# Performance work log

Hardware: AMD Instinct MI355X
Metric: run time of the kernel (lower is better)

The kernel has to match this reference:

```python
import jax, jax.numpy as jnp
import numpy as np

E = 100000          # number of edges
IN_FEATS = 256      # in_edge_feats
HIDDEN = 128        # hidden_size
K = 16              # neighbors per edge (uniform-degree rendering of ragged lists)


def setup_inputs() -> dict:
    key = jax.random.key(0)
    k1, k2, k3, k4 = jax.random.split(key, 4)
    edge_feats = jax.random.normal(k1, (E, IN_FEATS), dtype=jnp.float32)
    neighbors = jax.random.randint(k2, (E, K), 0, E, dtype=jnp.int32)
    # Linear params (torch Linear: y = x @ W^T + b; here W stored as [in, out])
    W = jax.random.normal(k3, (IN_FEATS, HIDDEN), dtype=jnp.float32) / np.sqrt(IN_FEATS)
    b = jax.random.normal(k4, (HIDDEN,), dtype=jnp.float32) * 0.01
    return {"edge_feats": edge_feats, "neighbors": neighbors, "W": W, "b": b}


def reference(edge_feats, neighbors, W, b):
    # Dense linear transform of all edge features: [E, H]
    t = edge_feats @ W + b
    # Gather each edge's K neighbor transformed features and sum: [E, K, H] -> [E, H]
    nbr_sum = jnp.take(t, neighbors, axis=0).sum(axis=1)
    # agg[i] = t[i] + sum_{n in neighbors[i]} t[n]
    return t + nbr_sum
```

## Files before the change

kernel.cpp:

```cpp
#include <hip/hip_runtime.h>
#include <hip/hip_bf16.h>
#include <stdint.h>

#define E_EDGES 100000
#define IN_F    256
#define HID     128
#define KNB     16

typedef short bf16x8 __attribute__((ext_vector_type(8)));
typedef float f32x4  __attribute__((ext_vector_type(4)));

__device__ __forceinline__ unsigned short f2bf(float f) {
    union { float f; unsigned u; } v; v.f = f;
    unsigned u = v.u;
    u += 0x7fffu + ((u >> 16) & 1u);
    return (unsigned short)(u >> 16);
}

__global__ void conv_w_kernel(const float* __restrict__ W, unsigned short* __restrict__ Wt) {
    int t = blockIdx.x * blockDim.x + threadIdx.x;
    int n = t & (HID - 1);
    int k = t >> 7;
    Wt[(size_t)n * IN_F + k] = f2bf(W[(size_t)k * HID + n]);
}

__launch_bounds__(256)
__global__ void gemm_t_kernel(const float* __restrict__ A,
                              const unsigned short* __restrict__ Wt,
                              const float* __restrict__ bias,
                              unsigned short* __restrict__ T) {
    const int wave = threadIdx.x >> 6;
    const int lane = threadIdx.x & 63;
    const int l15  = lane & 15;
    const int quad = lane >> 4;
    const int row0 = blockIdx.x * 32;
    const int col0 = wave * 32;

    f32x4 acc[2][2] = {};

    for (int k0 = 0; k0 < IN_F; k0 += 32) {
        bf16x8 afrag[2], bfrag[2];
        #pragma unroll
        for (int rt = 0; rt < 2; ++rt) {
            const float* ap = A + (size_t)(row0 + rt * 16 + l15) * IN_F + k0 + quad * 8;
            float4 lo = *(const float4*)ap;
            float4 hi = *(const float4*)(ap + 4);
            bf16x8 f;
            f[0] = (short)f2bf(lo.x); f[1] = (short)f2bf(lo.y);
            f[2] = (short)f2bf(lo.z); f[3] = (short)f2bf(lo.w);
            f[4] = (short)f2bf(hi.x); f[5] = (short)f2bf(hi.y);
            f[6] = (short)f2bf(hi.z); f[7] = (short)f2bf(hi.w);
            afrag[rt] = f;
        }
        #pragma unroll
        for (int ct = 0; ct < 2; ++ct) {
            const unsigned short* bp =
                Wt + (size_t)(col0 + ct * 16 + l15) * IN_F + k0 + quad * 8;
            bfrag[ct] = *(const bf16x8*)bp;
        }
        #pragma unroll
        for (int rt = 0; rt < 2; ++rt)
            #pragma unroll
            for (int ct = 0; ct < 2; ++ct)
                acc[rt][ct] = __builtin_amdgcn_mfma_f32_16x16x32_bf16(
                    afrag[rt], bfrag[ct], acc[rt][ct], 0, 0, 0);
    }

    #pragma unroll
    for (int rt = 0; rt < 2; ++rt) {
        #pragma unroll
        for (int ct = 0; ct < 2; ++ct) {
            const int col = col0 + ct * 16 + l15;
            const float bv = bias[col];
            #pragma unroll
            for (int i = 0; i < 4; ++i) {
                const int row = row0 + rt * 16 + quad * 4 + i;
                T[(size_t)row * HID + col] = f2bf(acc[rt][ct][i] + bv);
            }
        }
    }
}

__launch_bounds__(256)
__global__ void gather_sum_kernel(const unsigned short* __restrict__ T,
                                  const int* __restrict__ nbr,
                                  float* __restrict__ out) {
    __shared__ int sidx[256];
    const int tid   = threadIdx.x;
    const int edge0 = blockIdx.x * 16;
    sidx[tid] = nbr[(size_t)edge0 * KNB + tid];
    __syncthreads();

    const int el   = tid >> 4;
    const int lane = tid & 15;
    const int edge = edge0 + el;

    float acc[8];
    {
        uint4 v = *(const uint4*)(T + (size_t)edge * HID + lane * 8);
        unsigned w[4] = { v.x, v.y, v.z, v.w };
        union { unsigned u; float f; } c;
        #pragma unroll
        for (int j = 0; j < 4; ++j) {
            c.u = w[j] << 16;          acc[2 * j]     = c.f;
            c.u = w[j] & 0xffff0000u;  acc[2 * j + 1] = c.f;
        }
    }
    #pragma unroll
    for (int k = 0; k < KNB; ++k) {
        const int n = sidx[el * KNB + k];
        uint4 v = *(const uint4*)(T + (size_t)n * HID + lane * 8);
        unsigned w[4] = { v.x, v.y, v.z, v.w };
        union { unsigned u; float f; } c;
        #pragma unroll
        for (int j = 0; j < 4; ++j) {
            c.u = w[j] << 16;          acc[2 * j]     += c.f;
            c.u = w[j] & 0xffff0000u;  acc[2 * j + 1] += c.f;
        }
    }

    float* op = out + (size_t)edge * HID + lane * 8;
    float4 o0 = { acc[0], acc[1], acc[2], acc[3] };
    float4 o1 = { acc[4], acc[5], acc[6], acc[7] };
    *(float4*)op       = o0;
    *(float4*)(op + 4) = o1;
}

extern "C" void kernel_launch(void* const* d_in, const int* in_sizes, int n_in,
                              void* d_out, int out_size, void* d_ws, size_t ws_size,
                              hipStream_t stream) {
    const float* edge_feats = (const float*)d_in[0];
    const int*   neighbors  = (const int*)d_in[1];
    const float* W          = (const float*)d_in[2];
    const float* b          = (const float*)d_in[3];
    float*       out        = (float*)d_out;

    unsigned short* Wt = (unsigned short*)d_ws;
    unsigned short* T  = (unsigned short*)d_ws + (size_t)IN_F * HID;

    conv_w_kernel<<<(IN_F * HID) / 256, 256, 0, stream>>>(W, Wt);
    gemm_t_kernel<<<E_EDGES / 32, 256, 0, stream>>>(edge_feats, Wt, b, T);
    gather_sum_kernel<<<E_EDGES / 16, 256, 0, stream>>>(T, neighbors, out);
}
```

Before: 271.5 us.

## Restructure GEMM so each wave owns 16 rows across all columns, prefetching A

The GEMM tiling changes so that each wave computes a 16-row strip over all 128 output columns instead of a 32x32 tile. Every A element is now loaded and converted to bf16 exactly once rather than once per column-wave, and the whole A row slice is prefetched into registers up front to hide load latency. The cost is that each wave reads all of Wt, and the 16-entry float4 prefetch plus 8 accumulators raise register pressure. Bounds guards for the new 64-row block size are added.

```diff
diff --git a/kernel.cpp b/kernel.cpp
--- a/kernel.cpp
+++ b/kernel.cpp
@@ -33,50 +33,48 @@
     const int lane = threadIdx.x & 63;
     const int l15  = lane & 15;
     const int quad = lane >> 4;
-    const int row0 = blockIdx.x * 32;
-    const int col0 = wave * 32;
+    const int rowbase = blockIdx.x * 64 + wave * 16;
 
-    f32x4 acc[2][2] = {};
+    int arow = rowbase + l15;
+    if (arow >= E_EDGES) arow = E_EDGES - 1;
 
-    for (int k0 = 0; k0 < IN_F; k0 += 32) {
-        bf16x8 afrag[2], bfrag[2];
+    const float* ap = A + (size_t)arow * IN_F + quad * 8;
+    float4 apre[16];
+    #pragma unroll
+    for (int k0 = 0; k0 < 8; ++k0) {
+        apre[2 * k0]     = *(const float4*)(ap + k0 * 32);
+        apre[2 * k0 + 1] = *(const float4*)(ap + k0 * 32 + 4);
+    }
+
+    f32x4 acc[8] = {};
+
+    #pragma unroll
+    for (int k0 = 0; k0 < 8; ++k0) {
+        bf16x8 bfrag[8];
         #pragma unroll
-        for (int rt = 0; rt < 2; ++rt) {
-            const float* ap = A + (size_t)(row0 + rt * 16 + l15) * IN_F + k0 + quad * 8;
-            float4 lo = *(const float4*)ap;
-            float4 hi = *(const float4*)(ap + 4);
-            bf16x8 f;
-            f[0] = (short)f2bf(lo.x); f[1] = (short)f2bf(lo.y);
-            f[2] = (short)f2bf(lo.z); f[3] = (short)f2bf(lo.w);
-            f[4] = (short)f2bf(hi.x); f[5] = (short)f2bf(hi.y);
-            f[6] = (short)f2bf(hi.z); f[7] = (short)f2bf(hi.w);
-            afrag[rt] = f;
-        }
+        for (int ct = 0; ct < 8; ++ct)
+            bfrag[ct] = *(const bf16x8*)(Wt + (size_t)(ct * 16 + l15) * IN_F
+                                            + k0 * 32 + quad * 8);
+        float4 lo = apre[2 * k0], hi = apre[2 * k0 + 1];
+        bf16x8 af;
+        af[0] = (short)f2bf(lo.x); af[1] = (short)f2bf(lo.y);
+        af[2] = (short)f2bf(lo.z); af[3] = (short)f2bf(lo.w);
+        af[4] = (short)f2bf(hi.x); af[5] = (short)f2bf(hi.y);
+        af[6] = (short)f2bf(hi.z); af[7] = (short)f2bf(hi.w);
         #pragma unroll
-        for (int ct = 0; ct < 2; ++ct) {
-            const unsigned short* bp =
-                Wt + (size_t)(col0 + ct * 16 + l15) * IN_F + k0 + quad * 8;
-            bfrag[ct] = *(const bf16x8*)bp;
-        }
-        #pragma unroll
-        for (int rt = 0; rt < 2; ++rt)
-            #pragma unroll
-            for (int ct = 0; ct < 2; ++ct)
-                acc[rt][ct] = __builtin_amdgcn_mfma_f32_16x16x32_bf16(
-                    afrag[rt], bfrag[ct], acc[rt][ct], 0, 0, 0);
+        for (int ct = 0; ct < 8; ++ct)
+            acc[ct] = __builtin_amdgcn_mfma_f32_16x16x32_bf16(af, bfrag[ct], acc[ct], 0, 0, 0);
     }
 
     #pragma unroll
-    for (int rt = 0; rt < 2; ++rt) {
+    for (int ct = 0; ct < 8; ++ct) {
+        const int col = ct * 16 + l15;
+        const float bv = bias[col];
         #pragma unroll
-        for (int ct = 0; ct < 2; ++ct) {
-            const int col = col0 + ct * 16 + l15;
-            const float bv = bias[col];
-            #pragma unroll
-            for (int i = 0; i < 4; ++i) {
-                const int row = row0 + rt * 16 + quad * 4 + i;
-                T[(size_t)row * HID + col] = f2bf(acc[rt][ct][i] + bv);
-            }
+        for (int i = 0; i < 4; ++i) {
+            const int row = rowbase + quad * 4 + i;
+            if (row < E_EDGES)
+                T[(size_t)row * HID + col] = f2bf(acc[ct][i] + bv);
         }
     }
 }
@@ -139,6 +137,6 @@
     unsigned short* T  = (unsigned short*)d_ws + (size_t)IN_F * HID;
 
     conv_w_kernel<<<(IN_F * HID) / 256, 256, 0, stream>>>(W, Wt);
-    gemm_t_kernel<<<E_EDGES / 32, 256, 0, stream>>>(edge_feats, Wt, b, T);
+    gemm_t_kernel<<<(E_EDGES + 63) / 64, 256, 0, stream>>>(edge_feats, Wt, b, T);
     gather_sum_kernel<<<E_EDGES / 16, 256, 0, stream>>>(T, neighbors, out);
 }
```

New measurement: 268.4 us. No clear change (-1.1%).
